# Optimization experiments

Measured on AMD Instinct MI355X. Metric: run time of the kernel, lower is better.

## Reference

```python
import jax, jax.numpy as jnp
import numpy as np

# E8P 12-bit-abs codebook construction (faithful vectorized port of the torch code)
_SHUF = np.array([0, 2, 1, 3, 4, 6, 5, 7])  # shuffle_map
# get_norm12() * 2 (the integer matrix before the /2)
_NORM12_X2 = np.array([
    [3, 1, 1, 1, 3, 3, 3, 3], [1, 3, 1, 1, 3, 3, 3, 3], [1, 1, 3, 1, 3, 3, 3, 3],
    [1, 1, 1, 3, 3, 3, 3, 3], [3, 3, 3, 1, 3, 3, 1, 1], [3, 3, 3, 1, 3, 1, 3, 1],
    [3, 3, 3, 1, 1, 3, 3, 1], [3, 3, 3, 1, 3, 1, 1, 3], [3, 3, 3, 1, 1, 3, 1, 3],
    [3, 3, 3, 1, 1, 1, 3, 3], [3, 3, 1, 3, 3, 3, 1, 1], [3, 3, 1, 3, 3, 1, 3, 1],
    [3, 3, 1, 3, 1, 3, 3, 1], [3, 3, 1, 3, 3, 1, 1, 3], [3, 3, 1, 3, 1, 3, 1, 3],
    [3, 3, 1, 3, 1, 1, 3, 3], [3, 1, 3, 3, 3, 3, 1, 1], [3, 1, 3, 3, 3, 1, 3, 1],
    [3, 1, 3, 3, 1, 3, 3, 1], [3, 1, 3, 3, 3, 1, 1, 3], [3, 1, 3, 3, 1, 3, 1, 3],
    [1, 3, 3, 3, 1, 1, 3, 3], [1, 3, 3, 3, 3, 3, 1, 1], [1, 3, 3, 3, 3, 1, 3, 1],
    [1, 3, 3, 3, 1, 3, 3, 1], [1, 3, 3, 3, 3, 1, 1, 3], [1, 3, 3, 3, 1, 3, 1, 3],
    [1, 1, 3, 3, 1, 3, 3, 3], [3, 3, 1, 1, 3, 3, 3, 1]], dtype=np.int64)


def _packed_abs_grid():
    # Enumerate D8+1/2 lattice points, working with doubled integer coords (odd ints in [-7,7])
    idx = np.arange(8 ** 8, dtype=np.int64)
    cols, s, nrm = [], 0, 0
    for i in range(8):  # torch.cartesian_prod order: first dim varies slowest
        v = (2 * (((idx >> (3 * (7 - i))) & 7) - 4) + 1).astype(np.int8)  # 2*x for x in {-3.5..3.5}
        cols.append(v)
        w = v.astype(np.int32)
        s = s + w
        nrm = nrm + w * w
    mask = (s % 4 == 0) & (nrm <= 40)
    V = np.stack([c[mask] for c in cols], axis=1)
    d8abs2 = np.unique(np.abs(V), axis=0).astype(np.int64)  # lexsorted, doubled abs values
    cba2 = np.concatenate([d8abs2, _NORM12_X2], axis=0)[:, _SHUF]  # doubled values (== 2*cba)
    parity = (cba2.sum(1) // 2) % 2  # == cba.sum(1) % 2
    col = cba2 * 2  # == cba * 4, integer byte values in [2,14]
    col[:, 7] = col[:, 7] * (1 - 2 * parity)
    acc = np.zeros(col.shape[0], dtype=np.int64)
    for i in range(8):
        acc = acc | (col[:, i] << (8 * i))
    assert acc.shape[0] == 256
    return acc


def _full_grid():
    # Decode all 2^16 codes into the [65536, 8] fp32 codebook (port of get_full_grid)
    acc = _packed_abs_grid()
    c = np.arange(1 << 16, dtype=np.int64)
    signs = c & 255
    p = signs ^ (signs >> 4)
    p ^= p >> 2
    p ^= p >> 1
    parity = p & 1  # xor of the 8 sign bits
    signs = signs ^ parity
    ac = acc[c >> 8]  # packed abs code per entry
    byt = ((ac[:, None] >> (8 * _SHUF)) & 255).astype(np.uint8).astype(np.int8).astype(np.float32) / 4.0
    neg = ((signs[:, None] >> (7 - _SHUF)) & 1).astype(bool)
    vals = np.where(neg, -byt, byt) + np.where(parity[:, None] == 1, np.float32(-0.25), np.float32(0.25))
    return vals.astype(np.float32)


def setup_inputs() -> dict:
    key = jax.random.key(0)
    k1, k2 = jax.random.split(key)
    B = 4096          # tokens (batch * seq)
    M = 4096          # out_features = Qidxs rows
    N = 512           # Qidxs cols; in_features = N * 8 = 4096
    inp = jax.random.normal(k1, (B, N * 8), dtype=jnp.float32)
    Qidxs = jax.random.randint(k2, (M, N), 0, 1 << 16, dtype=jnp.int32)
    grid = jnp.asarray(_full_grid())  # [65536, 8] fp32 decoded E8P codebook
    return {"input": inp, "Qidxs": Qidxs, "grid": grid}


def reference(input, Qidxs, grid):
    m, n = Qidxs.shape
    # Dequantize: each int16 code indexes an 8-vector of the E8P codebook
    W = jnp.take(grid, Qidxs, axis=0).reshape(m, n * 8)  # [m, n*8] decompressed weight
    return input @ W.T  # [B, m]
```

## Files before the change

kernel.cpp:

```cpp
#include <hip/hip_runtime.h>
#include <hip/hip_bf16.h>

#define B_DIM 4096
#define M_DIM 4096
#define K_DIM 4096
#define NCODE 512

typedef __attribute__((ext_vector_type(4))) float f32x4;
typedef __attribute__((ext_vector_type(8))) short short8;

__device__ __forceinline__ unsigned short f2bf(float f) {
    union { float f; unsigned u; } c; c.f = f;
    unsigned u = c.u;
    return (unsigned short)((u + 0x7FFFu + ((u >> 16) & 1u)) >> 16);
}

__global__ __launch_bounds__(256) void dequant_kernel(const int* __restrict__ Q,
                                                      const float* __restrict__ cb,
                                                      short* __restrict__ Wout) {
    const int t = blockIdx.x * 256 + threadIdx.x;
    const int code = Q[t] & 0xFFFF;
    const float4* g = (const float4*)(cb + (size_t)code * 8);
    const float4 v0 = g[0];
    const float4 v1 = g[1];
    short8 o;
    o[0] = f2bf(v0.x); o[1] = f2bf(v0.y); o[2] = f2bf(v0.z); o[3] = f2bf(v0.w);
    o[4] = f2bf(v1.x); o[5] = f2bf(v1.y); o[6] = f2bf(v1.z); o[7] = f2bf(v1.w);
    *(short8*)(Wout + (size_t)t * 8) = o;
}

__global__ __launch_bounds__(256) void cvt_kernel(const float* __restrict__ in,
                                                  short* __restrict__ outb) {
    const int t = blockIdx.x * 256 + threadIdx.x;
    const float4* p = (const float4*)(in + (size_t)t * 8);
    const float4 v0 = p[0];
    const float4 v1 = p[1];
    short8 o;
    o[0] = f2bf(v0.x); o[1] = f2bf(v0.y); o[2] = f2bf(v0.z); o[3] = f2bf(v0.w);
    o[4] = f2bf(v1.x); o[5] = f2bf(v1.y); o[6] = f2bf(v1.z); o[7] = f2bf(v1.w);
    *(short8*)(outb + (size_t)t * 8) = o;
}

#define BM 256
#define BN 256
#define BK 32
#define NT (K_DIM / BK)

#define GLD(src, dst) \
    __builtin_amdgcn_global_load_lds( \
        (const __attribute__((address_space(1))) void*)(src), \
        (__attribute__((address_space(3))) void*)(dst), 16, 0, 0)

#define MFMA(a, b, c) __builtin_amdgcn_mfma_f32_16x16x32_bf16(a, b, c, 0, 0, 0)

__global__ __launch_bounds__(512, 2) void gemm_bt_kernel(const short* __restrict__ A,
                                                         const short* __restrict__ Wd,
                                                         float* __restrict__ C) {
    __shared__ short lds[4 * 16384];

    const int tid  = threadIdx.x;
    const int wave = tid >> 6;
    const int lane = tid & 63;

    const int bid = blockIdx.x;
    const int xcd = bid & 7;
    const int s   = bid >> 3;
    const int by  = (xcd >> 1) * 4 + (s >> 3);
    const int bx  = (xcd & 1) * 8 + (s & 7);

    const int rowBase = by * BM;
    const int colBase = bx * BN;

    const int wr = wave >> 2;
    const int wc = wave & 3;

    const int rA0 = tid >> 2;
    const int uu  = (tid & 3) ^ ((rA0 >> 1) & 3);
    const short* aSrc0 = A  + (size_t)(rowBase + rA0) * K_DIM + uu * 8;
    const short* aSrc1 = A  + (size_t)(rowBase + rA0 + 128) * K_DIM + uu * 8;
    const short* bSrc0 = Wd + (size_t)(colBase + rA0) * K_DIM + uu * 8;
    const short* bSrc1 = Wd + (size_t)(colBase + rA0 + 128) * K_DIM + uu * 8;

    const int l15 = lane & 15;
    const int l4  = lane >> 4;
    const int sx  = (l15 >> 1) & 3;
    const int aRd = (wr * 128 + l15) * 32 + (l4 ^ sx) * 8;
    const int bRd = 8192 + (wc * 64 + l15) * 32 + (l4 ^ sx) * 8;

    f32x4 acc[8][4] = {};
    short8 aX[4], bX[4], aY[4], bY[4], a1[4];

#pragma unroll
    for (int p = 0; p < 3; ++p) {
        const int koff = p * BK;
        short* base = &lds[p * 16384];
        GLD(aSrc0 + koff, base + wave * 512);
        GLD(aSrc1 + koff, base + 4096 + wave * 512);
        GLD(bSrc0 + koff, base + 8192 + wave * 512);
        GLD(bSrc1 + koff, base + 12288 + wave * 512);
    }
    asm volatile("s_waitcnt vmcnt(8)" ::: "memory");
    __builtin_amdgcn_s_barrier();
#pragma unroll
    for (int m = 0; m < 4; ++m) aX[m] = *(const short8*)&lds[aRd + m * 512];
#pragma unroll
    for (int n = 0; n < 4; ++n) bX[n] = *(const short8*)&lds[bRd + n * 512];

#define ITER_BODY(T, AC, BC, AN, BN)                                          \
    {                                                                         \
        const int buf    = ((T) & 3) * 16384;                                 \
        const int bufn   = (((T) + 1) & 3) * 16384;                           \
        const int tpre   = ((T) + 3 < NT) ? ((T) + 3) : (NT - 1);             \
        const int kpre   = tpre * BK;                                         \
        const int bufpre = (((T) + 3) & 3) * 16384;                           \
        _Pragma("unroll")                                                     \
        for (int m = 0; m < 4; ++m)                                           \
            a1[m] = *(const short8*)&lds[buf + aRd + (m + 4) * 512];          \
        GLD(aSrc0 + kpre, &lds[bufpre + wave * 512]);                         \
        GLD(aSrc1 + kpre, &lds[bufpre + 4096 + wave * 512]);                  \
        asm volatile("s_waitcnt vmcnt(6)" ::: "memory");                      \
        __builtin_amdgcn_s_barrier();                                         \
        __builtin_amdgcn_s_setprio(1);                                        \
        _Pragma("unroll")                                                     \
        for (int m = 0; m < 4; ++m)                                           \
            _Pragma("unroll")                                                 \
            for (int n = 0; n < 4; ++n)                                       \
                acc[m][n] = MFMA(AC[m], BC[n], acc[m][n]);                    \
        __builtin_amdgcn_s_setprio(0);                                        \
        GLD(bSrc0 + kpre, &lds[bufpre + 8192 + wave * 512]);                  \
        GLD(bSrc1 + kpre, &lds[bufpre + 12288 + wave * 512]);                 \
        asm volatile("s_waitcnt lgkmcnt(0)" ::: "memory");                    \
        __builtin_amdgcn_s_barrier();                                         \
        _Pragma("unroll")                                                     \
        for (int m = 0; m < 4; ++m)                                           \
            AN[m] = *(const short8*)&lds[bufn + aRd + m * 512];               \
        _Pragma("unroll")                                                     \
        for (int n = 0; n < 4; ++n)                                           \
            BN[n] = *(const short8*)&lds[bufn + bRd + n * 512];               \
        __builtin_amdgcn_s_setprio(1);                                        \
        _Pragma("unroll")                                                     \
        for (int m = 0; m < 4; ++m)                                           \
            _Pragma("unroll")                                                 \
            for (int n = 0; n < 4; ++n)                                       \
                acc[m + 4][n] = MFMA(a1[m], BC[n], acc[m + 4][n]);            \
        __builtin_amdgcn_s_setprio(0);                                        \
    }

    for (int t2 = 0; t2 < NT; t2 += 2) {
        ITER_BODY(t2,     aX, bX, aY, bY)
        ITER_BODY(t2 + 1, aY, bY, aX, bX)
    }
#undef ITER_BODY

    const int r0 = rowBase + wr * 128 + l4 * 4;
    const int c0 = colBase + wc * 64 + l15;
#pragma unroll
    for (int m = 0; m < 8; ++m)
#pragma unroll
        for (int n = 0; n < 4; ++n) {
            float* cp = C + (size_t)(r0 + m * 16) * M_DIM + (c0 + n * 16);
#pragma unroll
            for (int reg = 0; reg < 4; ++reg)
                cp[(size_t)reg * M_DIM] = acc[m][n][reg];
        }
}

extern "C" void kernel_launch(void* const* d_in, const int* in_sizes, int n_in,
                              void* d_out, int out_size, void* d_ws, size_t ws_size,
                              hipStream_t stream) {
    const float* inp  = (const float*)d_in[0];
    const int*   qidx = (const int*)d_in[1];
    const float* cb   = (const float*)d_in[2];
    float* out = (float*)d_out;

    short* Wb = (short*)d_ws;
    short* Ab = Wb + (size_t)M_DIM * K_DIM;

    const int n_codes = M_DIM * NCODE;
    dequant_kernel<<<n_codes / 256, 256, 0, stream>>>(qidx, cb, Wb);

    const int n_cvt = B_DIM * K_DIM / 8;
    cvt_kernel<<<n_cvt / 256, 256, 0, stream>>>(inp, Ab);

    gemm_bt_kernel<<<256, 512, 0, stream>>>(Ab, Wb, out);
}
```

Baseline: 141.9 us.

## Switch GEMM to 32x32x16 MFMA with 4 waves and fuse prep kernels

The GEMM now uses 32x32x16 bf16 MFMA instructions with 4 waves per block, each computing a 128x128 subtile, where before it used 16x16x32 MFMAs with 8 waves. The LDS read pattern, the load split across the two barriers and the epilogue store mapping are reworked to fit. The dequant and convert kernels are merged into one launch. The aim is fewer LDS reads per MFMA and one less launch, at the cost of higher register pressure per wave and fewer waves to hide latency.

After: 156.2 us. 1.1x slower.

```diff
diff --git a/kernel.cpp b/kernel.cpp
--- a/kernel.cpp
+++ b/kernel.cpp
@@ -7,6 +7,7 @@
 #define NCODE 512
 
 typedef __attribute__((ext_vector_type(4))) float f32x4;
+typedef __attribute__((ext_vector_type(16))) float f32x16;
 typedef __attribute__((ext_vector_type(8))) short short8;
 
 __device__ __forceinline__ unsigned short f2bf(float f) {
@@ -15,30 +16,32 @@
     return (unsigned short)((u + 0x7FFFu + ((u >> 16) & 1u)) >> 16);
 }
 
-__global__ __launch_bounds__(256) void dequant_kernel(const int* __restrict__ Q,
-                                                      const float* __restrict__ cb,
-                                                      short* __restrict__ Wout) {
-    const int t = blockIdx.x * 256 + threadIdx.x;
-    const int code = Q[t] & 0xFFFF;
-    const float4* g = (const float4*)(cb + (size_t)code * 8);
-    const float4 v0 = g[0];
-    const float4 v1 = g[1];
-    short8 o;
-    o[0] = f2bf(v0.x); o[1] = f2bf(v0.y); o[2] = f2bf(v0.z); o[3] = f2bf(v0.w);
-    o[4] = f2bf(v1.x); o[5] = f2bf(v1.y); o[6] = f2bf(v1.z); o[7] = f2bf(v1.w);
-    *(short8*)(Wout + (size_t)t * 8) = o;
-}
-
-__global__ __launch_bounds__(256) void cvt_kernel(const float* __restrict__ in,
-                                                  short* __restrict__ outb) {
-    const int t = blockIdx.x * 256 + threadIdx.x;
-    const float4* p = (const float4*)(in + (size_t)t * 8);
-    const float4 v0 = p[0];
-    const float4 v1 = p[1];
-    short8 o;
-    o[0] = f2bf(v0.x); o[1] = f2bf(v0.y); o[2] = f2bf(v0.z); o[3] = f2bf(v0.w);
-    o[4] = f2bf(v1.x); o[5] = f2bf(v1.y); o[6] = f2bf(v1.z); o[7] = f2bf(v1.w);
-    *(short8*)(outb + (size_t)t * 8) = o;
+__global__ __launch_bounds__(256) void prep_kernel(const int* __restrict__ Q,
+                                                   const float* __restrict__ cb,
+                                                   short* __restrict__ Wout,
+                                                   const float* __restrict__ in,
+                                                   short* __restrict__ Ab) {
+    const int b = blockIdx.x;
+    if (b < 8192) {
+        const int t = b * 256 + threadIdx.x;
+        const int code = Q[t] & 0xFFFF;
+        const float4* g = (const float4*)(cb + (size_t)code * 8);
+        const float4 v0 = g[0];
+        const float4 v1 = g[1];
+        short8 o;
+        o[0] = f2bf(v0.x); o[1] = f2bf(v0.y); o[2] = f2bf(v0.z); o[3] = f2bf(v0.w);
+        o[4] = f2bf(v1.x); o[5] = f2bf(v1.y); o[6] = f2bf(v1.z); o[7] = f2bf(v1.w);
+        *(short8*)(Wout + (size_t)t * 8) = o;
+    } else {
+        const int t = (b - 8192) * 256 + threadIdx.x;
+        const float4* p = (const float4*)(in + (size_t)t * 8);
+        const float4 v0 = p[0];
+        const float4 v1 = p[1];
+        short8 o;
+        o[0] = f2bf(v0.x); o[1] = f2bf(v0.y); o[2] = f2bf(v0.z); o[3] = f2bf(v0.w);
+        o[4] = f2bf(v1.x); o[5] = f2bf(v1.y); o[6] = f2bf(v1.z); o[7] = f2bf(v1.w);
+        *(short8*)(Ab + (size_t)t * 8) = o;
+    }
 }
 
 #define BM 256
@@ -51,9 +54,9 @@
         (const __attribute__((address_space(1))) void*)(src), \
         (__attribute__((address_space(3))) void*)(dst), 16, 0, 0)
 
-#define MFMA(a, b, c) __builtin_amdgcn_mfma_f32_16x16x32_bf16(a, b, c, 0, 0, 0)
-
-__global__ __launch_bounds__(512, 2) void gemm_bt_kernel(const short* __restrict__ A,
+#define MFMA32(a, b, c) __builtin_amdgcn_mfma_f32_32x32x16_bf16(a, b, c, 0, 0, 0)
+
+__global__ __launch_bounds__(256, 1) void gemm_bt_kernel(const short* __restrict__ A,
                                                          const short* __restrict__ Wd,
                                                          float* __restrict__ C) {
     __shared__ short lds[4 * 16384];
@@ -71,78 +74,102 @@
     const int rowBase = by * BM;
     const int colBase = bx * BN;
 
-    const int wr = wave >> 2;
-    const int wc = wave & 3;
+    const int wr = wave >> 1;
+    const int wc = wave & 1;
 
     const int rA0 = tid >> 2;
     const int uu  = (tid & 3) ^ ((rA0 >> 1) & 3);
-    const short* aSrc0 = A  + (size_t)(rowBase + rA0) * K_DIM + uu * 8;
-    const short* aSrc1 = A  + (size_t)(rowBase + rA0 + 128) * K_DIM + uu * 8;
-    const short* bSrc0 = Wd + (size_t)(colBase + rA0) * K_DIM + uu * 8;
-    const short* bSrc1 = Wd + (size_t)(colBase + rA0 + 128) * K_DIM + uu * 8;
-
-    const int l15 = lane & 15;
-    const int l4  = lane >> 4;
-    const int sx  = (l15 >> 1) & 3;
-    const int aRd = (wr * 128 + l15) * 32 + (l4 ^ sx) * 8;
-    const int bRd = 8192 + (wc * 64 + l15) * 32 + (l4 ^ sx) * 8;
-
-    f32x4 acc[8][4] = {};
-    short8 aX[4], bX[4], aY[4], bY[4], a1[4];
+    const size_t aIdx = (size_t)(rowBase + rA0) * K_DIM + uu * 8;
+    const size_t bIdx = (size_t)(colBase + rA0) * K_DIM + uu * 8;
+
+    const int l31 = lane & 31;
+    const int l5  = lane >> 5;
+    const int sx  = (l31 >> 1) & 3;
+    const int uk0 = ((l5)     ^ sx) * 8;
+    const int uk1 = ((l5 + 2) ^ sx) * 8;
+    const int aOff = (wr * 128 + l31) * 32;
+    const int bOff = 8192 + (wc * 128 + l31) * 32;
+
+    f32x16 acc[4][4] = {};
+    short8 aX[4], bX[8], aY[4], bY[8], a1[4];
 
 #pragma unroll
     for (int p = 0; p < 3; ++p) {
         const int koff = p * BK;
         short* base = &lds[p * 16384];
-        GLD(aSrc0 + koff, base + wave * 512);
-        GLD(aSrc1 + koff, base + 4096 + wave * 512);
-        GLD(bSrc0 + koff, base + 8192 + wave * 512);
-        GLD(bSrc1 + koff, base + 12288 + wave * 512);
-    }
-    asm volatile("s_waitcnt vmcnt(8)" ::: "memory");
+#pragma unroll
+        for (int c = 0; c < 4; ++c)
+            GLD(A + aIdx + koff + c * (64 * K_DIM), base + c * 2048 + wave * 512);
+#pragma unroll
+        for (int c = 0; c < 4; ++c)
+            GLD(Wd + bIdx + koff + c * (64 * K_DIM), base + 8192 + c * 2048 + wave * 512);
+    }
+    asm volatile("s_waitcnt vmcnt(16)" ::: "memory");
     __builtin_amdgcn_s_barrier();
 #pragma unroll
-    for (int m = 0; m < 4; ++m) aX[m] = *(const short8*)&lds[aRd + m * 512];
-#pragma unroll
-    for (int n = 0; n < 4; ++n) bX[n] = *(const short8*)&lds[bRd + n * 512];
-
-#define ITER_BODY(T, AC, BC, AN, BN)                                          \
+    for (int i = 0; i < 4; ++i)
+        aX[i] = *(const short8*)&lds[aOff + (i >> 1) * 1024 + ((i & 1) ? uk1 : uk0)];
+#pragma unroll
+    for (int j = 0; j < 8; ++j)
+        bX[j] = *(const short8*)&lds[bOff + (j >> 1) * 1024 + ((j & 1) ? uk1 : uk0)];
+
+#define ITER_BODY(T, AC, BC, AN, BN_)                                         \
     {                                                                         \
         const int buf    = ((T) & 3) * 16384;                                 \
         const int bufn   = (((T) + 1) & 3) * 16384;                           \
         const int tpre   = ((T) + 3 < NT) ? ((T) + 3) : (NT - 1);             \
         const int kpre   = tpre * BK;                                         \
         const int bufpre = (((T) + 3) & 3) * 16384;                           \
-        _Pragma("unroll")                                                     \
-        for (int m = 0; m < 4; ++m)                                           \
-            a1[m] = *(const short8*)&lds[buf + aRd + (m + 4) * 512];          \
-        GLD(aSrc0 + kpre, &lds[bufpre + wave * 512]);                         \
-        GLD(aSrc1 + kpre, &lds[bufpre + 4096 + wave * 512]);                  \
-        asm volatile("s_waitcnt vmcnt(6)" ::: "memory");                      \
+                \
+        _Pragma("unroll")                                                     \
+        for (int i = 0; i < 4; ++i)                                           \
+            a1[i] = *(const short8*)&lds[buf + aOff + (2 + (i >> 1)) * 1024 + \
+                                         ((i & 1) ? uk1 : uk0)];              \
+        _Pragma("unroll")                                                     \
+        for (int c = 0; c < 4; ++c)                                           \
+            GLD(A + aIdx + kpre + c * (64 * K_DIM),                           \
+                &lds[bufpre + c * 2048 + wave * 512]);                        \
+        asm volatile("s_waitcnt vmcnt(12)" ::: "memory");                     \
         __builtin_amdgcn_s_barrier();                                         \
+                             \
+        _Pragma("unroll")                                                     \
+        for (int j = 0; j < 6; ++j)                                           \
+            BN_[j] = *(const short8*)&lds[bufn + bOff + (j >> 1) * 1024 +     \
+                                          ((j & 1) ? uk1 : uk0)];             \
         __builtin_amdgcn_s_setprio(1);                                        \
         _Pragma("unroll")                                                     \
-        for (int m = 0; m < 4; ++m)                                           \
+        for (int ms = 0; ms < 2; ++ms)                                        \
             _Pragma("unroll")                                                 \
-            for (int n = 0; n < 4; ++n)                                       \
-                acc[m][n] = MFMA(AC[m], BC[n], acc[m][n]);                    \
+            for (int ns = 0; ns < 4; ++ns)                                    \
+                _Pragma("unroll")                                             \
+                for (int kk = 0; kk < 2; ++kk)                                \
+                    acc[ms][ns] = MFMA32(AC[ms * 2 + kk], BC[ns * 2 + kk],    \
+                                         acc[ms][ns]);                        \
         __builtin_amdgcn_s_setprio(0);                                        \
-        GLD(bSrc0 + kpre, &lds[bufpre + 8192 + wave * 512]);                  \
-        GLD(bSrc1 + kpre, &lds[bufpre + 12288 + wave * 512]);                 \
+        _Pragma("unroll")                                                     \
+        for (int c = 0; c < 4; ++c)                                           \
+            GLD(Wd + bIdx + kpre + c * (64 * K_DIM),                          \
+                &lds[bufpre + 8192 + c * 2048 + wave * 512]);                 \
         asm volatile("s_waitcnt lgkmcnt(0)" ::: "memory");                    \
         __builtin_amdgcn_s_barrier();                                         \
-        _Pragma("unroll")                                                     \
-        for (int m = 0; m < 4; ++m)                                           \
-            AN[m] = *(const short8*)&lds[bufn + aRd + m * 512];               \
-        _Pragma("unroll")                                                     \
-        for (int n = 0; n < 4; ++n)                                           \
-            BN[n] = *(const short8*)&lds[bufn + bRd + n * 512];               \
+                                \
+        _Pragma("unroll")                                                     \
+        for (int j = 6; j < 8; ++j)                                           \
+            BN_[j] = *(const short8*)&lds[bufn + bOff + (j >> 1) * 1024 +     \
+                                          ((j & 1) ? uk1 : uk0)];             \
+        _Pragma("unroll")                                                     \
+        for (int i = 0; i < 4; ++i)                                           \
+            AN[i] = *(const short8*)&lds[bufn + aOff + (i >> 1) * 1024 +      \
+                                         ((i & 1) ? uk1 : uk0)];              \
         __builtin_amdgcn_s_setprio(1);                                        \
         _Pragma("unroll")                                                     \
-        for (int m = 0; m < 4; ++m)                                           \
+        for (int ms = 0; ms < 2; ++ms)                                        \
             _Pragma("unroll")                                                 \
-            for (int n = 0; n < 4; ++n)                                       \
-                acc[m + 4][n] = MFMA(a1[m], BC[n], acc[m + 4][n]);            \
+            for (int ns = 0; ns < 4; ++ns)                                    \
+                _Pragma("unroll")                                             \
+                for (int kk = 0; kk < 2; ++kk)                                \
+                    acc[ms + 2][ns] = MFMA32(a1[ms * 2 + kk], BC[ns * 2 + kk],\
+                                             acc[ms + 2][ns]);                \
         __builtin_amdgcn_s_setprio(0);                                        \
     }
 
@@ -152,16 +179,18 @@
     }
 #undef ITER_BODY
 
-    const int r0 = rowBase + wr * 128 + l4 * 4;
-    const int c0 = colBase + wc * 64 + l15;
-#pragma unroll
-    for (int m = 0; m < 8; ++m)
-#pragma unroll
-        for (int n = 0; n < 4; ++n) {
-            float* cp = C + (size_t)(r0 + m * 16) * M_DIM + (c0 + n * 16);
-#pragma unroll
-            for (int reg = 0; reg < 4; ++reg)
-                cp[(size_t)reg * M_DIM] = acc[m][n][reg];
+    const int r0 = rowBase + wr * 128 + 4 * l5;
+    const int c0 = colBase + wc * 128 + l31;
+#pragma unroll
+    for (int ms = 0; ms < 4; ++ms)
+#pragma unroll
+        for (int ns = 0; ns < 4; ++ns) {
+            float* cp = C + (size_t)(r0 + ms * 32) * M_DIM + (c0 + ns * 32);
+#pragma unroll
+            for (int reg = 0; reg < 16; ++reg) {
+                const int rr = (reg & 3) + 8 * (reg >> 2);
+                cp[(size_t)rr * M_DIM] = acc[ms][ns][reg];
+            }
         }
 }
 
@@ -176,11 +205,7 @@
     short* Wb = (short*)d_ws;
     short* Ab = Wb + (size_t)M_DIM * K_DIM;
 
-    const int n_codes = M_DIM * NCODE;
-    dequant_kernel<<<n_codes / 256, 256, 0, stream>>>(qidx, cb, Wb);
-
-    const int n_cvt = B_DIM * K_DIM / 8;
-    cvt_kernel<<<n_cvt / 256, 256, 0, stream>>>(inp, Ab);
-
-    gemm_bt_kernel<<<256, 512, 0, stream>>>(Ab, Wb, out);
-}
+    prep_kernel<<<16384, 256, 0, stream>>>(qidx, cb, Wb, inp, Ab);
+
+    gemm_bt_kernel<<<256, 256, 0, stream>>>(Ab, Wb, out);
+}
```
